# Performance work log

Measured on AMD Instinct MI355X. Metric: run time of the kernel, lower is better.

The kernel has to match this reference:

```python
import jax, jax.numpy as jnp
import numpy as np

HEADS = 16
D_MODEL = 1024
D_K = D_MODEL // HEADS


def setup_inputs() -> dict:
    key = jax.random.key(0)
    ks = jax.random.split(key, 11)
    B, S, D = 4, 2048, D_MODEL
    q = jax.random.normal(ks[0], (B, S, D), dtype=jnp.float32)
    k = jax.random.normal(ks[1], (B, S, D), dtype=jnp.float32)
    v = jax.random.normal(ks[2], (B, S, D), dtype=jnp.float32)
    s = 1.0 / np.sqrt(D)
    Wq = jax.random.normal(ks[3], (D, D), dtype=jnp.float32) * s
    bq = jax.random.normal(ks[4], (D,), dtype=jnp.float32) * 0.01
    Wk = jax.random.normal(ks[5], (D, D), dtype=jnp.float32) * s
    bk = jax.random.normal(ks[6], (D,), dtype=jnp.float32) * 0.01
    Wv = jax.random.normal(ks[7], (D, D), dtype=jnp.float32) * s
    bv = jax.random.normal(ks[8], (D,), dtype=jnp.float32) * 0.01
    Wo = jax.random.normal(ks[9], (D, D), dtype=jnp.float32) * s
    bo = jax.random.normal(ks[10], (D,), dtype=jnp.float32) * 0.01
    return {"q": q, "k": k, "v": v, "Wq": Wq, "bq": bq, "Wk": Wk, "bk": bk,
            "Wv": Wv, "bv": bv, "Wo": Wo, "bo": bo}


def reference(q, k, v, Wq, bq, Wk, bk, Wv, bv, Wo, bo):
    B, Sq, D = q.shape
    Sk = k.shape[1]
    # Linear projections (torch Linear: x @ W.T + b)
    q_ = (q @ Wq.T + bq).reshape(B, Sq, HEADS, D_K).transpose(0, 2, 1, 3)  # [B,H,Sq,Dk]
    k_ = (k @ Wk.T + bk).reshape(B, Sk, HEADS, D_K).transpose(0, 2, 1, 3)  # [B,H,Sk,Dk]
    v_ = (v @ Wv.T + bv).reshape(B, Sk, HEADS, D_K).transpose(0, 2, 1, 3)  # [B,H,Sk,Dk]
    scores = jnp.einsum("bhqd,bhkd->bhqk", q_, k_) / jnp.sqrt(jnp.float32(D_K))
    attn = jax.nn.softmax(scores, axis=-1)
    ctx = jnp.einsum("bhqk,bhkd->bhqd", attn, v_)  # [B,H,Sq,Dk]
    concat = ctx.transpose(0, 2, 1, 3).reshape(B, Sq, D)
    # dropout p=0 -> identity (eval)
    return concat @ Wo.T + bo
```

## Files before the change

kernel.cpp:

```cpp
#include <hip/hip_runtime.h>
#include <hip/hip_bf16.h>
#include <stdint.h>

typedef unsigned short u16;
typedef __attribute__((ext_vector_type(8))) short bf16x8;
typedef __attribute__((ext_vector_type(4))) float f32x4;
typedef __attribute__((ext_vector_type(16))) float f32x16;
typedef __attribute__((ext_vector_type(4))) int i32x4;

#define BATCH 4
#define HEADS 16
#define SEQ   2048
#define DMODEL 1024
#define DK    64
#define QSCALE (0.125f * 1.44269504088896340736f)

__device__ __forceinline__ u16 f2bf(float f) {
  __hip_bfloat16 h = __float2bfloat16(f);
  return *reinterpret_cast<u16*>(&h);
}

__device__ __forceinline__ int cvtpk(float a, float b) {
  int r;
  asm("v_cvt_pk_bf16_f32 %0, %1, %2" : "=v"(r) : "v"(a), "v"(b));
  return r;
}

__device__ __forceinline__ void plswap(int& a, int& b) {
  asm volatile("v_permlane32_swap_b32 %0, %1" : "+v"(a), "+v"(b));
}

__device__ __forceinline__ void gload_lds16(const u16* g, u16* l) {
  __builtin_amdgcn_global_load_lds((const __attribute__((address_space(1))) void*)g,
                                   (__attribute__((address_space(3))) void*)l, 16, 0, 0);
}

__device__ __forceinline__ void sbar() {
  asm volatile("" ::: "memory");
  __builtin_amdgcn_s_barrier();
  __builtin_amdgcn_sched_barrier(0);
}
#define WAITV(N)                                              \
  do {                                                        \
    asm volatile("s_waitcnt vmcnt(" #N ")" ::: "memory");     \
    __builtin_amdgcn_sched_barrier(0);                        \
  } while (0)
#define WAITLGKM0()                                           \
  do {                                                        \
    asm volatile("s_waitcnt lgkmcnt(0)" ::: "memory");        \
    __builtin_amdgcn_sched_barrier(0);                        \
  } while (0)

__global__ void cvt_w(const float* __restrict__ w0, const float* __restrict__ w1,
                      const float* __restrict__ w2, const float* __restrict__ w3,
                      u16* __restrict__ o0, u16* __restrict__ o1,
                      u16* __restrict__ o2, u16* __restrict__ o3) {
  const int sel = blockIdx.y;
  long i = ((long)blockIdx.x * blockDim.x + threadIdx.x) * 8;
  const float* in = (sel == 0) ? w0 : (sel == 1) ? w1 : (sel == 2) ? w2 : w3;
  u16* out = (sel == 0) ? o0 : (sel == 1) ? o1 : (sel == 2) ? o2 : o3;
  float4 a = *(const float4*)(in + i);
  float4 b = *(const float4*)(in + i + 4);
  i32x4 pk;
  pk[0] = cvtpk(a.x, a.y); pk[1] = cvtpk(a.z, a.w);
  pk[2] = cvtpk(b.x, b.y); pk[3] = cvtpk(b.z, b.w);
  *(i32x4*)(out + i) = pk;
}

__global__ __launch_bounds__(256, 4)
void gemm97_qkv(const float* __restrict__ qf, const float* __restrict__ kf,
                const float* __restrict__ vf, const u16* __restrict__ Wqb,
                const u16* __restrict__ Wkb, const u16* __restrict__ Wvb,
                const float* __restrict__ bq, const float* __restrict__ bk,
                const float* __restrict__ bv, u16* __restrict__ Qp,
                u16* __restrict__ Kp, u16* __restrict__ Vt) {
  __shared__ __align__(16) u16 smem[20480];
  u16* As = smem;
  u16* Bs = smem + 8192;
  const int K = DMODEL;
  const int tid = threadIdx.x;
  const int lane = tid & 63;
  const int w = tid >> 6;
  const int wm = w >> 1, wn = w & 1;
  const int lr = lane & 15, lg = lane >> 4;

  const int wg = blockIdx.y * 24 + blockIdx.x;
  const int swz = (wg & 7) * 192 + (wg >> 3);
  const int bcolg = swz % 24;
  const int brow = swz / 24;
  const int sel = bcolg >> 3;
  const int bcol = bcolg & 7;

  const float* Ag = ((sel == 0) ? qf : (sel == 1) ? kf : vf) + (size_t)(brow * 128) * K;
  const u16* Bg = ((sel == 0) ? Wqb : (sel == 1) ? Wkb : Wvb) + (size_t)(bcol * 128) * K;
  const float* bias = (sel == 0) ? bq : (sel == 1) ? bk : bv;

  const int r0_ = tid >> 2;
  const int c0_ = (((tid & 3) ^ (r0_ & 3)) * 8);
  const int c1_ = (((tid & 3) ^ ((r0_ + 64) & 3)) * 8);

  f32x4 acc[4][4] = {};
  float4 areg[2][2];

  areg[0][0] = *(const float4*)(Ag + (size_t)r0_ * K + c0_);
  areg[0][1] = *(const float4*)(Ag + (size_t)r0_ * K + c0_ + 4);
  areg[1][0] = *(const float4*)(Ag + (size_t)(r0_ + 64) * K + c1_);
  areg[1][1] = *(const float4*)(Ag + (size_t)(r0_ + 64) * K + c1_ + 4);
#pragma unroll
  for (int j = 0; j < 2; j++) {
    i32x4 pk;
    pk[0] = cvtpk(areg[j][0].x, areg[j][0].y);
    pk[1] = cvtpk(areg[j][0].z, areg[j][0].w);
    pk[2] = cvtpk(areg[j][1].x, areg[j][1].y);
    pk[3] = cvtpk(areg[j][1].z, areg[j][1].w);
    *(i32x4*)(As + (tid + j * 256) * 8) = pk;
  }
  gload_lds16(Bg + (size_t)r0_ * K + c0_, Bs + tid * 8);
  gload_lds16(Bg + (size_t)(r0_ + 64) * K + c1_, Bs + (tid + 256) * 8);
  gload_lds16(Bg + (size_t)r0_ * K + 32 + c0_, Bs + 4096 + tid * 8);
  gload_lds16(Bg + (size_t)(r0_ + 64) * K + 32 + c1_, Bs + 4096 + (tid + 256) * 8);
  areg[0][0] = *(const float4*)(Ag + (size_t)r0_ * K + 32 + c0_);
  areg[0][1] = *(const float4*)(Ag + (size_t)r0_ * K + 32 + c0_ + 4);
  areg[1][0] = *(const float4*)(Ag + (size_t)(r0_ + 64) * K + 32 + c1_);
  areg[1][1] = *(const float4*)(Ag + (size_t)(r0_ + 64) * K + 32 + c1_ + 4);
  WAITV(6);
  WAITLGKM0();
  sbar();

  const int NT = 32;
  int bcur = 0;
  for (int t = 0; t < NT; ++t) {
    const int p = t & 1;
    const u16* Ab = As + p * 4096;
    const u16* Bb = Bs + bcur * 4096;

    if (t + 1 < NT) {
      u16* Ad = As + (p ^ 1) * 4096;
#pragma unroll
      for (int j = 0; j < 2; j++) {
        i32x4 pk;
        pk[0] = cvtpk(areg[j][0].x, areg[j][0].y);
        pk[1] = cvtpk(areg[j][0].z, areg[j][0].w);
        pk[2] = cvtpk(areg[j][1].x, areg[j][1].y);
        pk[3] = cvtpk(areg[j][1].z, areg[j][1].w);
        *(i32x4*)(Ad + (tid + j * 256) * 8) = pk;
      }
      if (t + 2 < NT) {
        const int k2 = (t + 2) * 32;
        areg[0][0] = *(const float4*)(Ag + (size_t)r0_ * K + k2 + c0_);
        areg[0][1] = *(const float4*)(Ag + (size_t)r0_ * K + k2 + c0_ + 4);
        areg[1][0] = *(const float4*)(Ag + (size_t)(r0_ + 64) * K + k2 + c1_);
        areg[1][1] = *(const float4*)(Ag + (size_t)(r0_ + 64) * K + k2 + c1_ + 4);
        const int bn2 = (bcur + 2 >= 3) ? bcur - 1 : bcur + 2;
        u16* Bd = Bs + bn2 * 4096;
        gload_lds16(Bg + (size_t)r0_ * K + k2 + c0_, Bd + tid * 8);
        gload_lds16(Bg + (size_t)(r0_ + 64) * K + k2 + c1_, Bd + (tid + 256) * 8);
      }
      __builtin_amdgcn_sched_barrier(0);
    }

    bf16x8 a[4], b[4];
#pragma unroll
    for (int i = 0; i < 4; i++) {
      const int r = wm * 64 + i * 16 + lr;
      a[i] = *(const bf16x8*)&Ab[r * 32 + ((lg ^ (r & 3)) * 8)];
    }
#pragma unroll
    for (int j = 0; j < 4; j++) {
      const int r = wn * 64 + j * 16 + lr;
      b[j] = *(const bf16x8*)&Bb[r * 32 + ((lg ^ (r & 3)) * 8)];
    }
    __builtin_amdgcn_s_setprio(1);
#pragma unroll
    for (int i = 0; i < 4; i++)
#pragma unroll
      for (int j = 0; j < 4; j++)
        acc[i][j] = __builtin_amdgcn_mfma_f32_16x16x32_bf16(a[i], b[j], acc[i][j], 0, 0, 0);
    __builtin_amdgcn_s_setprio(0);

    if (t + 2 < NT) {
      WAITV(6);
    } else {
      WAITV(0);
    }
    WAITLGKM0();
    sbar();
    bcur = (bcur + 1 >= 3) ? 0 : bcur + 1;
  }

  if (sel < 2) {
    u16* Cout = (sel == 0) ? Qp : Kp;
    const float oscale = (sel == 0) ? QSCALE : 1.f;
#pragma unroll
    for (int j = 0; j < 4; j++) {
      const int col = bcol * 128 + wn * 64 + j * 16 + lr;
      const float bv_ = bias[col];
#pragma unroll
      for (int i = 0; i < 4; i++) {
        const int row0 = brow * 128 + wm * 64 + i * 16 + lg * 4;
#pragma unroll
        for (int r = 0; r < 4; r++)
          Cout[(size_t)(row0 + r) * DMODEL + col] = f2bf((acc[i][j][r] + bv_) * oscale);
      }
    }
  } else {
    const int b = brow >> 4;
    const int s0 = (brow & 15) * 128;
    u16* tr = smem;
    __syncthreads();
#pragma unroll
    for (int j = 0; j < 4; j++) {
      const int col = wn * 64 + j * 16 + lr;
      const int xsw = (col & 7) << 3;
      const float bv_ = bias[bcol * 128 + col];
#pragma unroll
      for (int i = 0; i < 4; i++) {
        const int rr0 = wm * 64 + i * 16 + lg * 4;
#pragma unroll
        for (int pr = 0; pr < 2; pr++) {
          const float e0 = acc[i][j][pr * 2] + bv_;
          const float e1 = acc[i][j][pr * 2 + 1] + bv_;
          *(int*)&tr[col * 128 + ((rr0 + pr * 2) ^ xsw)] = cvtpk(e0, e1);
        }
      }
    }
    __syncthreads();
    const int col = tid >> 1;
    const int part = tid & 1;
    const int xsw = (col & 7) << 3;
    const int c = bcol * 128 + col;
    const int hh = c >> 6, dk = c & 63;
    u16* dst = Vt + (size_t)((b * 16 + hh) * 64 + dk) * SEQ + s0 + part * 64;
#pragma unroll
    for (int jj = 0; jj < 8; jj++) {
      bf16x8 vv = *(const bf16x8*)&tr[col * 128 + ((part * 64 + jj * 8) ^ xsw)];
      *(bf16x8*)(dst + jj * 8) = vv;
    }
  }
}

__device__ __forceinline__ void gemm_kloop(
    const u16* __restrict__ Ag, const u16* __restrict__ Bg,
    u16* As, u16* Bs, f32x4 acc[4][4],
    const int tid, const int wm, const int wn, const int lr, const int lg) {
  const int K = DMODEL;
  int arow[4], acolc[4], brow2[2], bcol2[2];
#pragma unroll
  for (int j = 0; j < 4; j++) {
    const int c = tid + j * 512;
    arow[j] = c >> 3;
    acolc[j] = ((c & 7) ^ (arow[j] & 7)) * 8;
  }
#pragma unroll
  for (int j = 0; j < 2; j++) {
    const int c = tid + j * 512;
    brow2[j] = c >> 3;
    bcol2[j] = ((c & 7) ^ (brow2[j] & 7)) * 8;
  }

#pragma unroll
  for (int j = 0; j < 4; j++)
    gload_lds16(Ag + (size_t)arow[j] * K + acolc[j], As + (tid + j * 512) * 8);
#pragma unroll
  for (int j = 0; j < 2; j++)
    gload_lds16(Bg + (size_t)brow2[j] * K + bcol2[j], Bs + (tid + j * 512) * 8);
#pragma unroll
  for (int j = 0; j < 4; j++)
    gload_lds16(Ag + (size_t)arow[j] * K + 64 + acolc[j], As + 16384 + (tid + j * 512) * 8);
#pragma unroll
  for (int j = 0; j < 2; j++)
    gload_lds16(Bg + (size_t)brow2[j] * K + 64 + bcol2[j], Bs + 8192 + (tid + j * 512) * 8);
  WAITV(6);
  sbar();

  int m = 0;
  for (int t = 0; t < 16; ++t) {
    u16* Ab = As + m * 16384;
    u16* Bb = Bs + (t & 1) * 8192;
    const int m2 = (m + 2 >= 3) ? m - 1 : m + 2;
    const int k1 = (t + 1) * 64;
    const int k2 = (t + 2) * 64;

    bf16x8 a[4], b[4];
#pragma unroll
    for (int i = 0; i < 4; i++) {
      const int r = wm * 64 + i * 16 + lr;
      a[i] = *(const bf16x8*)&Ab[r * 64 + ((lg ^ (r & 7)) * 8)];
    }
#pragma unroll
    for (int j = 0; j < 4; j++) {
      const int r = wn * 64 + j * 16 + lr;
      b[j] = *(const bf16x8*)&Bb[r * 64 + ((lg ^ (r & 7)) * 8)];
    }
    if (t + 1 < 16) {
      u16* Bd = Bs + ((t + 1) & 1) * 8192;
      gload_lds16(Bg + (size_t)brow2[0] * K + k1 + bcol2[0], Bd + tid * 8);
      gload_lds16(Bg + (size_t)brow2[1] * K + k1 + bcol2[1], Bd + (tid + 512) * 8);
    }
    if (t + 2 < 16) {
      u16* Ad = As + m2 * 16384;
      gload_lds16(Ag + (size_t)arow[0] * K + k2 + acolc[0], Ad + tid * 8);
      gload_lds16(Ag + (size_t)arow[1] * K + k2 + acolc[1], Ad + (tid + 512) * 8);
    }
    sbar();
    __builtin_amdgcn_s_setprio(1);
#pragma unroll
    for (int i = 0; i < 4; i++)
#pragma unroll
      for (int j = 0; j < 4; j++)
        acc[i][j] = __builtin_amdgcn_mfma_f32_16x16x32_bf16(a[i], b[j], acc[i][j], 0, 0, 0);
    __builtin_amdgcn_s_setprio(0);
    sbar();

#pragma unroll
    for (int i = 0; i < 4; i++) {
      const int r = wm * 64 + i * 16 + lr;
      a[i] = *(const bf16x8*)&Ab[r * 64 + (((4 + lg) ^ (r & 7)) * 8)];
    }
#pragma unroll
    for (int j = 0; j < 4; j++) {
      const int r = wn * 64 + j * 16 + lr;
      b[j] = *(const bf16x8*)&Bb[r * 64 + (((4 + lg) ^ (r & 7)) * 8)];
    }
    if (t + 2 < 16) {
      u16* Ad = As + m2 * 16384;
      gload_lds16(Ag + (size_t)arow[2] * K + k2 + acolc[2], Ad + (tid + 1024) * 8);
      gload_lds16(Ag + (size_t)arow[3] * K + k2 + acolc[3], Ad + (tid + 1536) * 8);
    }
    sbar();
    __builtin_amdgcn_s_setprio(1);
#pragma unroll
    for (int i = 0; i < 4; i++)
#pragma unroll
      for (int j = 0; j < 4; j++)
        acc[i][j] = __builtin_amdgcn_mfma_f32_16x16x32_bf16(a[i], b[j], acc[i][j], 0, 0, 0);
    __builtin_amdgcn_s_setprio(0);
    if (t < 14) {
      WAITV(4);
    } else {
      WAITV(0);
    }
    sbar();
    m = (m + 1 >= 3) ? 0 : m + 1;
  }
}

__global__ __launch_bounds__(512, 2)
void gemm8_bt(const u16* __restrict__ A, const u16* __restrict__ Bm,
              const float* __restrict__ bias, float* __restrict__ Cout) {
  __shared__ __align__(16) u16 smem[65536];
  u16* As = smem;
  u16* Bs = smem + 49152;
  const int tid = threadIdx.x;
  const int lane = tid & 63;
  const int w = tid >> 6;
  const int wm = w >> 1, wn = w & 1;
  const int lr = lane & 15, lg = lane >> 4;

  const int wg = blockIdx.y * 8 + blockIdx.x;
  const int swz = (wg & 7) * 32 + (wg >> 3);
  const int bcol = swz & 7;
  const int brow = swz >> 3;

  f32x4 acc[4][4] = {};
  gemm_kloop(A + (size_t)(brow * 256) * DMODEL, Bm + (size_t)(bcol * 128) * DMODEL,
             As, Bs, acc, tid, wm, wn, lr, lg);

#pragma unroll
  for (int j = 0; j < 4; j++) {
    const int col = bcol * 128 + wn * 64 + j * 16 + lr;
    const float bv_ = bias[col];
#pragma unroll
    for (int i = 0; i < 4; i++) {
      const int row0 = brow * 256 + wm * 64 + i * 16 + lg * 4;
#pragma unroll
      for (int r = 0; r < 4; r++)
        Cout[(size_t)(row0 + r) * DMODEL + col] = acc[i][j][r] + bv_;
    }
  }
}

__device__ __forceinline__ void pack_group(const float* p, int* pw) {
  int W0 = cvtpk(p[0], p[1]);
  int W1 = cvtpk(p[2], p[3]);
  int W2 = cvtpk(p[4], p[5]);
  int W3 = cvtpk(p[6], p[7]);
  plswap(W0, W2);
  plswap(W1, W3);
  pw[0] = W0; pw[1] = W1; pw[2] = W2; pw[3] = W3;
}

__global__ __launch_bounds__(256, 4)
void attn2(const u16* __restrict__ Qp, const u16* __restrict__ Kp,
           const u16* __restrict__ Vt, u16* __restrict__ ctx) {
  __shared__ __align__(16) u16 smem[16384];
  const int tid = threadIdx.x;
  const int lane = tid & 63, w = tid >> 6;
  const int hi = lane >> 5;
  const int l31 = lane & 31;

  const int wg = blockIdx.y * gridDim.x + blockIdx.x;
  const int swz = (wg & 7) * 128 + (wg >> 3);
  const int bh = swz >> 4;
  const int b = bh >> 4, h = bh & 15;
  const int q0 = (swz & 15) * 128 + w * 32;

  const u16* qrow = Qp + (size_t)(b * SEQ + q0 + l31) * DMODEL + h * DK + hi * 8;
  bf16x8 qf[4];
#pragma unroll
  for (int kk = 0; kk < 4; kk++) qf[kk] = *(const bf16x8*)(qrow + kk * 16);

  const int srow = tid >> 3;
  const int scb = tid & 7;
  const int scol = (scb ^ (srow & 7)) * 8;
  const u16* kp = Kp + (size_t)(b * SEQ + srow) * DMODEL + h * DK + scol;
  const u16* vp = Vt + (size_t)bh * DK * SEQ + (size_t)srow * SEQ + scol;

  const int ksw = (l31 & 7) << 3;

  f32x16 o0 = {}, o1 = {};
  float lacc[4] = {};
  const int NT = SEQ / 64;

  {
    u16* Kd = smem;
    u16* Vd = smem + 4096;
    gload_lds16(kp, Kd + tid * 8);
    gload_lds16(kp + 32 * DMODEL, Kd + tid * 8 + 2048);
    gload_lds16(vp, Vd + tid * 8);
    gload_lds16(vp + 32 * SEQ, Vd + tid * 8 + 2048);
    kp += 64 * DMODEL;
    vp += 64;
  }
  __syncthreads();

  for (int t = 0; t < NT; ++t) {
    const int p = t & 1;
    if (t + 1 < NT) {
      u16* Kd = smem + ((p ^ 1) << 13);
      u16* Vd = Kd + 4096;
      gload_lds16(kp, Kd + tid * 8);
      gload_lds16(kp + 32 * DMODEL, Kd + tid * 8 + 2048);
      gload_lds16(vp, Vd + tid * 8);
      gload_lds16(vp + 32 * SEQ, Vd + tid * 8 + 2048);
      kp += 64 * DMODEL;
      vp += 64;
    }

    const u16* Kc = smem + (p << 13);
    const u16* Vc = Kc + 4096;

    f32x16 st0 = {}, st1 = {};
    __builtin_amdgcn_s_setprio(1);
#pragma unroll
    for (int kk = 0; kk < 4; kk++) {
      const int slot = (((kk * 2 + hi) << 3) ^ ksw);
      bf16x8 k0 = *(const bf16x8*)&Kc[l31 * 64 + slot];
      bf16x8 k1 = *(const bf16x8*)&Kc[(l31 + 32) * 64 + slot];
      st0 = __builtin_amdgcn_mfma_f32_32x32x16_bf16(k0, qf[kk], st0, 0, 0, 0);
      st1 = __builtin_amdgcn_mfma_f32_32x32x16_bf16(k1, qf[kk], st1, 0, 0, 0);
    }
    __builtin_amdgcn_s_setprio(0);

#pragma unroll
    for (int i = 0; i < 16; i++) st0[i] = __builtin_amdgcn_exp2f(st0[i]);
#pragma unroll
    for (int i = 0; i < 16; i++) st1[i] = __builtin_amdgcn_exp2f(st1[i]);
    float ts[8];
#pragma unroll
    for (int i = 0; i < 8; i++) ts[i] = (st0[i] + st0[i + 8]) + (st1[i] + st1[i + 8]);
#pragma unroll
    for (int i = 0; i < 4; i++) lacc[i] += ts[i] + ts[i + 4];

    int pw[4][4];
    {
      float tmp[8];
#pragma unroll
      for (int i = 0; i < 8; i++) tmp[i] = st0[i];
      pack_group(tmp, pw[0]);
#pragma unroll
      for (int i = 0; i < 8; i++) tmp[i] = st0[i + 8];
      pack_group(tmp, pw[1]);
#pragma unroll
      for (int i = 0; i < 8; i++) tmp[i] = st1[i];
      pack_group(tmp, pw[2]);
#pragma unroll
      for (int i = 0; i < 8; i++) tmp[i] = st1[i + 8];
      pack_group(tmp, pw[3]);
    }

    __builtin_amdgcn_s_setprio(1);
#pragma unroll
    for (int c = 0; c < 4; c++) {
      i32x4 pwv;
      pwv[0] = pw[c][0]; pwv[1] = pw[c][1]; pwv[2] = pw[c][2]; pwv[3] = pw[c][3];
      bf16x8 pf = __builtin_bit_cast(bf16x8, pwv);
      const int slot = (((c * 2 + hi) << 3) ^ ksw);
      bf16x8 v0 = *(const bf16x8*)&Vc[l31 * 64 + slot];
      bf16x8 v1 = *(const bf16x8*)&Vc[(l31 + 32) * 64 + slot];
      o0 = __builtin_amdgcn_mfma_f32_32x32x16_bf16(v0, pf, o0, 0, 0, 0);
      o1 = __builtin_amdgcn_mfma_f32_32x32x16_bf16(v1, pf, o1, 0, 0, 0);
    }
    __builtin_amdgcn_s_setprio(0);

    __syncthreads();
  }

  float lsum = (lacc[0] + lacc[1]) + (lacc[2] + lacc[3]);
  lsum += __shfl_xor(lsum, 32);
  const float rl = 1.0f / lsum;
  u16* ot = smem + w * (32 * 72);
#pragma unroll
  for (int ds_ = 0; ds_ < 2; ds_++) {
#pragma unroll
    for (int g = 0; g < 4; g++) {
#pragma unroll
      for (int pr = 0; pr < 2; pr++) {
        const int r = g * 4 + pr * 2;
        const int d = ds_ * 32 + (r & 3) + 8 * (r >> 2) + 4 * hi;
        float e0 = (ds_ ? o1[r] : o0[r]) * rl;
        float e1 = (ds_ ? o1[r + 1] : o0[r + 1]) * rl;
        *(int*)&ot[l31 * 72 + d] = cvtpk(e0, e1);
      }
    }
  }
  __syncthreads();
  const int rq = lane >> 3;
  const int rc = (lane & 7) * 8;
#pragma unroll
  for (int it = 0; it < 4; ++it) {
    const int qq = it * 8 + rq;
    bf16x8 vrow = *(const bf16x8*)&ot[qq * 72 + rc];
    *(bf16x8*)&ctx[(size_t)(b * SEQ + q0 + qq) * DMODEL + h * DK + rc] = vrow;
  }
}

extern "C" void kernel_launch(void* const* d_in, const int* in_sizes, int n_in,
                              void* d_out, int out_size, void* d_ws, size_t ws_size,
                              hipStream_t stream) {
  const float* q  = (const float*)d_in[0];
  const float* k  = (const float*)d_in[1];
  const float* v  = (const float*)d_in[2];
  const float* Wq = (const float*)d_in[3];
  const float* bq = (const float*)d_in[4];
  const float* Wk = (const float*)d_in[5];
  const float* bk = (const float*)d_in[6];
  const float* Wv = (const float*)d_in[7];
  const float* bv = (const float*)d_in[8];
  const float* Wo = (const float*)d_in[9];
  const float* bo = (const float*)d_in[10];

  char* ws = (char*)d_ws;
  const size_t MB = 1024 * 1024;
  u16* Wqb = (u16*)(ws + 48 * MB);
  u16* Wkb = (u16*)(ws + 50 * MB);
  u16* Wvb = (u16*)(ws + 52 * MB);
  u16* Wob = (u16*)(ws + 54 * MB);
  u16* Qp  = (u16*)(ws + 56 * MB);
  u16* Kp  = (u16*)(ws + 72 * MB);
  u16* Vt  = (u16*)(ws + 104 * MB);
  u16* ctx = (u16*)(ws + 120 * MB);

  const long nW = (long)DMODEL * DMODEL;

  cvt_w<<<dim3(nW / 8 / 256, 4), 256, 0, stream>>>(Wq, Wk, Wv, Wo, Wqb, Wkb, Wvb, Wob);

  gemm97_qkv<<<dim3(24, 64), 256, 0, stream>>>(q, k, v, Wqb, Wkb, Wvb,
                                               bq, bk, bv, Qp, Kp, Vt);

  attn2<<<dim3(16, 64), 256, 0, stream>>>(Qp, Kp, Vt, ctx);

  gemm8_bt<<<dim3(8, 32), 512, 0, stream>>>(ctx, Wob, bo, (float*)d_out);
}
```

Baseline: 189.0 us.

## Load K/V tiles directly from global memory into registers, dropping LDS staging

The attention kernel no longer stages K and V tiles through double-buffered shared memory with async global-to-LDS loads and per-tile barriers. Each wave now reads its MFMA operands straight from global memory into registers every iteration, and shared memory is kept only for the output transpose. This removes LDS traffic and the block-wide syncs, but each of the four waves now fetches the same K/V data separately (a fourfold increase in global/L2 reads). It also loses the explicit prefetch overlap, so load latency is exposed unless the compiler hoists the loads.

```diff
diff --git a/kernel.cpp b/kernel.cpp
--- a/kernel.cpp
+++ b/kernel.cpp
@@ -391,9 +391,9 @@
 }
 
 __global__ __launch_bounds__(256, 4)
-void attn2(const u16* __restrict__ Qp, const u16* __restrict__ Kp,
+void attn3(const u16* __restrict__ Qp, const u16* __restrict__ Kp,
            const u16* __restrict__ Vt, u16* __restrict__ ctx) {
-  __shared__ __align__(16) u16 smem[16384];
+  __shared__ __align__(16) u16 ot_s[4 * 32 * 72];
   const int tid = threadIdx.x;
   const int lane = tid & 63, w = tid >> 6;
   const int hi = lane >> 5;
@@ -410,55 +410,38 @@
 #pragma unroll
   for (int kk = 0; kk < 4; kk++) qf[kk] = *(const bf16x8*)(qrow + kk * 16);
 
-  const int srow = tid >> 3;
-  const int scb = tid & 7;
-  const int scol = (scb ^ (srow & 7)) * 8;
-  const u16* kp = Kp + (size_t)(b * SEQ + srow) * DMODEL + h * DK + scol;
-  const u16* vp = Vt + (size_t)bh * DK * SEQ + (size_t)srow * SEQ + scol;
-
-  const int ksw = (l31 & 7) << 3;
+  const u16* kpA = Kp + (size_t)(b * SEQ + l31) * DMODEL + h * DK + hi * 8;
+  const u16* kpB = kpA + (size_t)32 * DMODEL;
+  const u16* vpA = Vt + ((size_t)bh * DK + l31) * SEQ + hi * 8;
+  const u16* vpB = vpA + (size_t)32 * SEQ;
 
   f32x16 o0 = {}, o1 = {};
   float lacc[4] = {};
   const int NT = SEQ / 64;
 
-  {
-    u16* Kd = smem;
-    u16* Vd = smem + 4096;
-    gload_lds16(kp, Kd + tid * 8);
-    gload_lds16(kp + 32 * DMODEL, Kd + tid * 8 + 2048);
-    gload_lds16(vp, Vd + tid * 8);
-    gload_lds16(vp + 32 * SEQ, Vd + tid * 8 + 2048);
-    kp += 64 * DMODEL;
-    vp += 64;
-  }
-  __syncthreads();
-
   for (int t = 0; t < NT; ++t) {
-    const int p = t & 1;
-    if (t + 1 < NT) {
-      u16* Kd = smem + ((p ^ 1) << 13);
-      u16* Vd = Kd + 4096;
-      gload_lds16(kp, Kd + tid * 8);
-      gload_lds16(kp + 32 * DMODEL, Kd + tid * 8 + 2048);
-      gload_lds16(vp, Vd + tid * 8);
-      gload_lds16(vp + 32 * SEQ, Vd + tid * 8 + 2048);
-      kp += 64 * DMODEL;
-      vp += 64;
-    }
-
-    const u16* Kc = smem + (p << 13);
-    const u16* Vc = Kc + 4096;
+    bf16x8 kA[4], kB[4], vA[4], vB[4];
+#pragma unroll
+    for (int kk = 0; kk < 4; kk++) {
+      kA[kk] = *(const bf16x8*)(kpA + kk * 16);
+      kB[kk] = *(const bf16x8*)(kpB + kk * 16);
+    }
+#pragma unroll
+    for (int c = 0; c < 4; c++) {
+      vA[c] = *(const bf16x8*)(vpA + c * 16);
+      vB[c] = *(const bf16x8*)(vpB + c * 16);
+    }
+    kpA += 64 * DMODEL;
+    kpB += 64 * DMODEL;
+    vpA += 64;
+    vpB += 64;
 
     f32x16 st0 = {}, st1 = {};
     __builtin_amdgcn_s_setprio(1);
 #pragma unroll
     for (int kk = 0; kk < 4; kk++) {
-      const int slot = (((kk * 2 + hi) << 3) ^ ksw);
-      bf16x8 k0 = *(const bf16x8*)&Kc[l31 * 64 + slot];
-      bf16x8 k1 = *(const bf16x8*)&Kc[(l31 + 32) * 64 + slot];
-      st0 = __builtin_amdgcn_mfma_f32_32x32x16_bf16(k0, qf[kk], st0, 0, 0, 0);
-      st1 = __builtin_amdgcn_mfma_f32_32x32x16_bf16(k1, qf[kk], st1, 0, 0, 0);
+      st0 = __builtin_amdgcn_mfma_f32_32x32x16_bf16(kA[kk], qf[kk], st0, 0, 0, 0);
+      st1 = __builtin_amdgcn_mfma_f32_32x32x16_bf16(kB[kk], qf[kk], st1, 0, 0, 0);
     }
     __builtin_amdgcn_s_setprio(0);
 
@@ -495,21 +478,16 @@
       i32x4 pwv;
       pwv[0] = pw[c][0]; pwv[1] = pw[c][1]; pwv[2] = pw[c][2]; pwv[3] = pw[c][3];
       bf16x8 pf = __builtin_bit_cast(bf16x8, pwv);
-      const int slot = (((c * 2 + hi) << 3) ^ ksw);
-      bf16x8 v0 = *(const bf16x8*)&Vc[l31 * 64 + slot];
-      bf16x8 v1 = *(const bf16x8*)&Vc[(l31 + 32) * 64 + slot];
-      o0 = __builtin_amdgcn_mfma_f32_32x32x16_bf16(v0, pf, o0, 0, 0, 0);
-      o1 = __builtin_amdgcn_mfma_f32_32x32x16_bf16(v1, pf, o1, 0, 0, 0);
+      o0 = __builtin_amdgcn_mfma_f32_32x32x16_bf16(vA[c], pf, o0, 0, 0, 0);
+      o1 = __builtin_amdgcn_mfma_f32_32x32x16_bf16(vB[c], pf, o1, 0, 0, 0);
     }
     __builtin_amdgcn_s_setprio(0);
-
-    __syncthreads();
   }
 
   float lsum = (lacc[0] + lacc[1]) + (lacc[2] + lacc[3]);
   lsum += __shfl_xor(lsum, 32);
   const float rl = 1.0f / lsum;
-  u16* ot = smem + w * (32 * 72);
+  u16* ot = ot_s + w * (32 * 72);
 #pragma unroll
   for (int ds_ = 0; ds_ < 2; ds_++) {
 #pragma unroll
@@ -568,7 +546,7 @@
   gemm97_qkv<<<dim3(24, 64), 256, 0, stream>>>(q, k, v, Wqb, Wkb, Wvb,
                                                bq, bk, bv, Qp, Kp, Vt);
 
-  attn2<<<dim3(16, 64), 256, 0, stream>>>(Qp, Kp, Vt, ctx);
+  attn3<<<dim3(16, 64), 256, 0, stream>>>(Qp, Kp, Vt, ctx);
 
   gemm8_bt<<<dim3(8, 32), 512, 0, stream>>>(ctx, Wob, bo, (float*)d_out);
 }
```

After: 392.2 us. 108% more time.
